# Optimization experiments

Hardware: AMD Instinct MI355X
Metric: run time of the kernel (lower is better)

Reference implementation:

```python
import jax, jax.numpy as jnp
import numpy as np

N, E, F_IN, H, EF, G, GFD = 50000, 800000, 64, 128, 8, 10, 2
NEG_SLOPE = 0.2  # PyG GATv2Conv default negative_slope


def _gatv2_layer(x, src, dst, edge_attr, Wl, bl, Wr, br, We, att, bias):
    # PyG GATv2Conv, heads=1, concat=True, share_weights=False
    n = x.shape[0]
    xl = x @ Wl + bl            # source transform [N,H]
    xr = x @ Wr + br            # target transform [N,H]
    e = edge_attr @ We          # edge embedding   [E,H]
    s = jax.nn.leaky_relu(xl[src] + xr[dst] + e, NEG_SLOPE)  # [E,H]
    logits = s @ att            # [E]
    # numerically-stable segment softmax over destination nodes
    mx = jax.ops.segment_max(logits, dst, num_segments=n)
    mx = jnp.where(jnp.isfinite(mx), mx, 0.0)
    ex = jnp.exp(logits - mx[dst])
    den = jax.ops.segment_sum(ex, dst, num_segments=n)
    alpha = ex / jnp.maximum(den[dst], 1e-16)
    out = jax.ops.segment_sum(alpha[:, None] * xl[src], dst, num_segments=n)
    return out + bias


def _forward(x, edge_index, edge_attr, graph_features, num_graphs, params, head_W, head_b):
    src, dst = edge_index[0], edge_index[1]
    for (Wl, bl, Wr, br, We, att, bias) in params:
        x = jax.nn.relu(_gatv2_layer(x, src, dst, edge_attr, Wl, bl, Wr, br, We, att, bias))
        # dropout p=0.0 / eval mode: no-op
    n_nodes = x.shape[0] // num_graphs
    # faithful replication of the torch reshape chain (graph_feature_dim == 2):
    # graph_features.T [GFD,G] -> unsqueeze(2) -> repeat to [GFD,G,Np] -> view(G,GFD,Np)
    # -> cat(unbind(0), dim=1) -> [GFD, G*Np]
    gf = jnp.broadcast_to(graph_features.T[:, :, None], (GFD, num_graphs, n_nodes))
    gf = gf.reshape(num_graphs, GFD, n_nodes)
    gf = gf.transpose(1, 0, 2).reshape(GFD, num_graphs * n_nodes)
    x = jnp.concatenate([x, gf.T], axis=1)  # [N, H+GFD]
    return x @ head_W + head_b


def setup_inputs():
    key = jax.random.key(0)
    ks = list(jax.random.split(key, 32))
    p = lambda k, s: jax.random.normal(k, s, jnp.float32) * 0.05
    inp = {
        'x': jax.random.normal(ks[0], (N, F_IN), jnp.float32),
        'edge_index': jax.random.randint(ks[1], (2, E), 0, N),
        'edge_attr': jax.random.normal(ks[2], (E, EF), jnp.float32),
        'graph_features': jax.random.normal(ks[3], (G, GFD), jnp.float32),
        'num_graphs': G,
    }
    i = 4
    for l in range(3):
        fin = F_IN if l == 0 else H
        inp[f'Wl{l}'] = p(ks[i], (fin, H)); i += 1
        inp[f'bl{l}'] = jnp.zeros((H,), jnp.float32)
        inp[f'Wr{l}'] = p(ks[i], (fin, H)); i += 1
        inp[f'br{l}'] = jnp.zeros((H,), jnp.float32)
        inp[f'We{l}'] = p(ks[i], (EF, H)); i += 1
        inp[f'att{l}'] = p(ks[i], (H,)); i += 1
        inp[f'bias{l}'] = jnp.zeros((H,), jnp.float32)
    inp['head_W'] = p(ks[i], (H + GFD, 1))
    inp['head_b'] = jnp.zeros((1,), jnp.float32)
    return inp


def reference(x, edge_index, edge_attr, graph_features, num_graphs,
              Wl0, bl0, Wr0, br0, We0, att0, bias0,
              Wl1, bl1, Wr1, br1, We1, att1, bias1,
              Wl2, bl2, Wr2, br2, We2, att2, bias2,
              head_W, head_b):
    params = [(Wl0, bl0, Wr0, br0, We0, att0, bias0),
              (Wl1, bl1, Wr1, br1, We1, att1, bias1),
              (Wl2, bl2, Wr2, br2, We2, att2, bias2)]
    return _forward(x, edge_index, edge_attr, graph_features, num_graphs, params, head_W, head_b)
```

## Files before the change

kernel.cpp:

```cpp
#include <hip/hip_runtime.h>
#include <hip/hip_bf16.h>
#include <math.h>

#define NN 50000
#define EE 800000
#define F_IN 64
#define HH 128
#define EF 8
#define GG 10
#define GFD 2
#define NEG_SLOPE 0.2f
#define NB 64

typedef float v2f __attribute__((ext_vector_type(2)));
__device__ __forceinline__ v2f fma2(v2f a, v2f b, v2f c) {
  return __builtin_elementwise_fma(a, b, c);
}
__device__ __forceinline__ v2f bc2(float x) { v2f r; r.x = x; r.y = x; return r; }

__device__ __forceinline__ float lrelu1(float x) {
  return fmaxf(x, NEG_SLOPE * x);
}

template <int CTRL>
__device__ __forceinline__ float dpp_add(float v) {
  int p = __builtin_amdgcn_update_dpp(0, __float_as_int(v), CTRL, 0xf, 0xf, true);
  return v + __int_as_float(p);
}
__device__ __forceinline__ float red32(float v) {
  v = dpp_add<0xB1>(v);
  v = dpp_add<0x4E>(v);
  v = dpp_add<0x141>(v);
  v = dpp_add<0x140>(v);
  v += __int_as_float(__builtin_amdgcn_ds_swizzle(__float_as_int(v), 0x401F));
  return v;
}

__device__ __forceinline__ void lin2_body(
    int bid, const float* __restrict__ x, int fin,
    const float* __restrict__ Wl, const float* __restrict__ bl,
    const float* __restrict__ Wr, const float* __restrict__ br,
    float* __restrict__ xl, float* __restrict__ xr, int n_nodes) {
  __shared__ float xs[64 * 128];
  const int tid = threadIdx.x;
  const int base = bid * 64;
  int nrows = n_nodes - base; if (nrows > 64) nrows = 64;

  const int total4 = (nrows * fin) >> 2;
  const float4* xsrc = (const float4*)(x + (size_t)base * fin);
  float4* xd = (float4*)xs;
  for (int i = tid; i < total4; i += 256) xd[i] = xsrc[i];
  __syncthreads();

  const int lane = tid & 63;
  const int w = tid >> 6;
  const int c = lane * 2;

  float accl0[16], accl1[16], accr0[16], accr1[16];
#pragma unroll
  for (int j = 0; j < 16; j++) { accl0[j]=0.f; accl1[j]=0.f; accr0[j]=0.f; accr1[j]=0.f; }

  const float* xrow = xs + (w * 16) * fin;
  for (int k = 0; k < fin; k += 4) {
    float2 wl0 = *(const float2*)(Wl + (size_t)k * HH + c);
    float2 wl1 = *(const float2*)(Wl + (size_t)(k + 1) * HH + c);
    float2 wl2 = *(const float2*)(Wl + (size_t)(k + 2) * HH + c);
    float2 wl3 = *(const float2*)(Wl + (size_t)(k + 3) * HH + c);
    float2 wr0 = *(const float2*)(Wr + (size_t)k * HH + c);
    float2 wr1 = *(const float2*)(Wr + (size_t)(k + 1) * HH + c);
    float2 wr2 = *(const float2*)(Wr + (size_t)(k + 2) * HH + c);
    float2 wr3 = *(const float2*)(Wr + (size_t)(k + 3) * HH + c);
#pragma unroll
    for (int j = 0; j < 16; j++) {
      float4 xv = *(const float4*)(xrow + j * fin + k);
      accl0[j] = fmaf(xv.x, wl0.x, accl0[j]);
      accl1[j] = fmaf(xv.x, wl0.y, accl1[j]);
      accr0[j] = fmaf(xv.x, wr0.x, accr0[j]);
      accr1[j] = fmaf(xv.x, wr0.y, accr1[j]);
      accl0[j] = fmaf(xv.y, wl1.x, accl0[j]);
      accl1[j] = fmaf(xv.y, wl1.y, accl1[j]);
      accr0[j] = fmaf(xv.y, wr1.x, accr0[j]);
      accr1[j] = fmaf(xv.y, wr1.y, accr1[j]);
      accl0[j] = fmaf(xv.z, wl2.x, accl0[j]);
      accl1[j] = fmaf(xv.z, wl2.y, accl1[j]);
      accr0[j] = fmaf(xv.z, wr2.x, accr0[j]);
      accr1[j] = fmaf(xv.z, wr2.y, accr1[j]);
      accl0[j] = fmaf(xv.w, wl3.x, accl0[j]);
      accl1[j] = fmaf(xv.w, wl3.y, accl1[j]);
      accr0[j] = fmaf(xv.w, wr3.x, accr0[j]);
      accr1[j] = fmaf(xv.w, wr3.y, accr1[j]);
    }
  }
  float2 blv = *(const float2*)(bl + c);
  float2 brv = *(const float2*)(br + c);
#pragma unroll
  for (int j = 0; j < 16; j++) {
    int n = base + w * 16 + j;
    if (n < n_nodes) {
      *(float2*)(xl + (size_t)n * HH + c) = make_float2(accl0[j] + blv.x, accl1[j] + blv.y);
      *(float2*)(xr + (size_t)n * HH + c) = make_float2(accr0[j] + brv.x, accr1[j] + brv.y);
    }
  }
}

__global__ __launch_bounds__(256) void lin2_kernel(
    const float* __restrict__ x, int fin,
    const float* __restrict__ Wl, const float* __restrict__ bl,
    const float* __restrict__ Wr, const float* __restrict__ br,
    float* __restrict__ xl, float* __restrict__ xr, int n_nodes) {
  lin2_body(blockIdx.x, x, fin, Wl, bl, Wr, br, xl, xr, n_nodes);
}

__device__ __forceinline__ void hist_body(int bid, const int* __restrict__ dst,
                                          int* __restrict__ hist, int ne) {
  int i = bid * 256 + threadIdx.x;
  if (i < ne) atomicAdd(&hist[dst[i]], 1);
}

__global__ __launch_bounds__(256) void fusedA_kernel(
    int nl2, const float* __restrict__ x, int fin,
    const float* __restrict__ Wl, const float* __restrict__ bl,
    const float* __restrict__ Wr, const float* __restrict__ br,
    float* __restrict__ xl, float* __restrict__ xr, int n_nodes,
    const int* __restrict__ dst, int* __restrict__ hist, int ne) {
  if ((int)blockIdx.x < nl2)
    lin2_body(blockIdx.x, x, fin, Wl, bl, Wr, br, xl, xr, n_nodes);
  else
    hist_body(blockIdx.x - nl2, dst, hist, ne);
}

__global__ __launch_bounds__(1024) void reduce_kernel(const int* __restrict__ hist,
                                                      int* __restrict__ bsum, int n) {
  __shared__ int wsum[16];
  const int tid = threadIdx.x;
  const int lane = tid & 63, w = tid >> 6;
  int i = blockIdx.x * 1024 + tid;
  int v = (i < n) ? hist[i] : 0;
#pragma unroll
  for (int off = 32; off; off >>= 1) v += __shfl_xor(v, off);
  if (lane == 0) wsum[w] = v;
  __syncthreads();
  if (tid < 16) {
    int s = wsum[tid];
#pragma unroll
    for (int off = 8; off; off >>= 1) s += __shfl_xor(s, off);
    if (tid == 0) bsum[blockIdx.x] = s;
  }
}

__global__ __launch_bounds__(64) void scanb_kernel(const int* __restrict__ bsum,
                                                   int* __restrict__ bbase,
                                                   int* __restrict__ offs, int nb, int n) {
  const int tid = threadIdx.x;
  int v = (tid < nb) ? bsum[tid] : 0;
  int inc = v;
#pragma unroll
  for (int d = 1; d < 64; d <<= 1) {
    int t2 = __shfl_up(inc, d);
    if (tid >= d) inc += t2;
  }
  if (tid < nb) bbase[tid] = inc - v;
  if (tid == 63) offs[n] = inc;
}

__global__ __launch_bounds__(1024) void scanc_kernel(const int* __restrict__ hist,
                                                     const int* __restrict__ bbase,
                                                     int* __restrict__ offs,
                                                     int* __restrict__ cursor, int n) {
  __shared__ int wsum[16], wpre[16];
  const int tid = threadIdx.x;
  const int lane = tid & 63, w = tid >> 6;
  int i = blockIdx.x * 1024 + tid;
  int orig = (i < n) ? hist[i] : 0;
  int v = orig;
#pragma unroll
  for (int d = 1; d < 64; d <<= 1) {
    int t2 = __shfl_up(v, d);
    if (lane >= d) v += t2;
  }
  if (lane == 63) wsum[w] = v;
  __syncthreads();
  if (tid < 16) {
    int s = wsum[tid];
    int inc = s;
#pragma unroll
    for (int d = 1; d < 16; d <<= 1) {
      int t2 = __shfl_up(inc, d);
      if (tid >= d) inc += t2;
    }
    wpre[tid] = inc - s;
  }
  __syncthreads();
  if (i < n) {
    int ex = bbase[blockIdx.x] + wpre[w] + (v - orig);
    offs[i] = ex; cursor[i] = ex;
  }
}

__device__ __forceinline__ void scatter_body(
    int bid, const int* __restrict__ src, const int* __restrict__ dst,
    int* __restrict__ cursor, int* __restrict__ pk,
    const float4* __restrict__ ea4, float4* __restrict__ eas, int ne) {
  int i = bid * 256 + threadIdx.x;
  if (i < ne) {
    int d = dst[i];
    int pos = atomicAdd(&cursor[d], 1);
    pk[pos] = src[i] * 512;
    float4 a = ea4[i * 2], b = ea4[i * 2 + 1];
    eas[pos * 2] = a; eas[pos * 2 + 1] = b;
  }
}

__device__ __forceinline__ void deg_hist_body(int bid, const int* __restrict__ offs,
                                              int* __restrict__ hist2, int n) {
  __shared__ int lhist[NB];
  const int tid = threadIdx.x;
  int i = bid * 256 + tid;
  if (tid < NB) lhist[tid] = 0;
  __syncthreads();
  if (i < n) {
    int d = offs[i + 1] - offs[i];
    int key = NB - 1 - min(d, NB - 1);
    atomicAdd(&lhist[key], 1);
  }
  __syncthreads();
  if (tid < NB && lhist[tid]) atomicAdd(&hist2[tid], lhist[tid]);
}

__global__ __launch_bounds__(256) void fusedB_kernel(
    int nsc, const int* __restrict__ src, const int* __restrict__ dst,
    int* __restrict__ cursor, int* __restrict__ pk,
    const float4* __restrict__ ea4, float4* __restrict__ eas, int ne,
    const int* __restrict__ offs, int* __restrict__ hist2, int n) {
  if ((int)blockIdx.x < nsc)
    scatter_body(blockIdx.x, src, dst, cursor, pk, ea4, eas, ne);
  else
    deg_hist_body(blockIdx.x - nsc, offs, hist2, n);
}

__global__ __launch_bounds__(64) void scan64_kernel(const int* __restrict__ hist2,
                                                    int* __restrict__ cursor2) {
  const int tid = threadIdx.x;
  int v = hist2[tid];
  int inc = v;
#pragma unroll
  for (int d = 1; d < 64; d <<= 1) {
    int t2 = __shfl_up(inc, d);
    if (tid >= d) inc += t2;
  }
  cursor2[tid] = inc - v;
}

__global__ __launch_bounds__(256) void deg_scatter_kernel(const int* __restrict__ offs,
                                                          int* __restrict__ cursor2,
                                                          int4* __restrict__ meta4, int n) {
  __shared__ int lhist[NB];
  __shared__ int lbase[NB];
  const int tid = threadIdx.x;
  int i = blockIdx.x * 256 + tid;
  if (tid < NB) lhist[tid] = 0;
  __syncthreads();
  int key = 0, rank = 0, bb = 0, ee = 0;
  const bool valid = (i < n);
  if (valid) {
    bb = offs[i]; ee = offs[i + 1];
    int d = ee - bb;
    key = NB - 1 - min(d, NB - 1);
    rank = atomicAdd(&lhist[key], 1);
  }
  __syncthreads();
  if (tid < NB && lhist[tid]) lbase[tid] = atomicAdd(&cursor2[tid], lhist[tid]);
  __syncthreads();
  if (valid) meta4[lbase[key] + rank] = make_int4(bb, ee, i, 0);
}

__global__ __launch_bounds__(256, 4) void gat_fused_kernel(
    const float* __restrict__ xl, const float* __restrict__ xr,
    const float* __restrict__ eas, const float* __restrict__ We,
    const float* __restrict__ att,
    const int* __restrict__ pk, const int4* __restrict__ meta4,
    const float* __restrict__ bias,
    float* __restrict__ xout, int n_nodes,
    float* __restrict__ out_head, const float* __restrict__ hw,
    const float* __restrict__ hb) {
  const int lane = threadIdx.x & 63;
  const int g = lane >> 5, t = lane & 31;
  const int c = t * 4;
  const int tb = t * 16;
  const int nwaves = gridDim.x * 4;

  v2f wea[EF], web[EF];
#pragma unroll
  for (int k = 0; k < EF; k++) {
    float4 w4 = *(const float4*)(We + k * HH + c);
    wea[k].x = w4.x; wea[k].y = w4.y;
    web[k].x = w4.z; web[k].y = w4.w;
  }
  const float4 at = *(const float4*)(att + c);
  const float4 bi = *(const float4*)(bias + c);
  const char* xlb = (const char*)xl;
  const char* easb = (const char*)eas;
  float4 hwv = make_float4(0.f, 0.f, 0.f, 0.f);
  float hw0 = 0.f, hw1 = 0.f, hb0 = 0.f;
  if (out_head) {
    hwv = *(const float4*)(hw + c);
    hw0 = hw[HH]; hw1 = hw[HH + 1]; hb0 = hb[0];
  }

  int wid = blockIdx.x * 4 + (threadIdx.x >> 6);
  if (wid >= n_nodes) return;
  int4 mt = meta4[wid];
  float4 vr4 = *(const float4*)(xr + (size_t)mt.z * HH + c);

  while (true) {
    const int b = mt.x, e = mt.y, node = mt.z;
    const int deg = e - b;
    const int nwid = wid + nwaves;
    const bool hasN = nwid < n_nodes;
    int4 mtN = mt;
    if (hasN) mtN = meta4[nwid];

    v2f vra; vra.x = vr4.x; vra.y = vr4.y;
    v2f vrb; vrb.x = vr4.z; vrb.y = vr4.w;

    float4 o;
    if (deg == 0) {
      o.x = fmaxf(bi.x, 0.f); o.y = fmaxf(bi.y, 0.f);
      o.z = fmaxf(bi.z, 0.f); o.w = fmaxf(bi.w, 0.f);
    } else {
      const int emax = e - 1;
      v2f acc0 = bc2(0.f), acc1 = bc2(0.f);
      float den = 0.f;
      v2f vlAa, vlAb, epA0, epA1, eqA0, eqA1;
      v2f vlBa, vlBb, epB0, epB1, eqB0, eqB1;

#define LOADS(VLa, VLb, P0, P1, Q0, Q1, IDX)                        \
  do {                                                              \
    int _cx = min((IDX), emax);                                     \
    float4 _ep = *(const float4*)(easb + (_cx << 5));               \
    float4 _eq = *(const float4*)(easb + (_cx << 5) + 16);          \
    int _ob = pk[_cx];                                              \
    float4 _vl = *(const float4*)(xlb + (_ob + tb));                \
    P0.x = _ep.x; P0.y = _ep.y; P1.x = _ep.z; P1.y = _ep.w;         \
    Q0.x = _eq.x; Q0.y = _eq.y; Q1.x = _eq.z; Q1.y = _eq.w;         \
    VLa.x = _vl.x; VLa.y = _vl.y; VLb.x = _vl.z; VLb.y = _vl.w;     \
  } while (0)

#define PROCESS(VLa, VLb, P0, P1, Q0, Q1, IDX)                       \
  do {                                                               \
    v2f s0 = VLa + vra;                                              \
    v2f s1 = VLb + vrb;                                              \
    s0 = fma2(bc2(P0.x), wea[0], s0); s1 = fma2(bc2(P0.x), web[0], s1); \
    s0 = fma2(bc2(P0.y), wea[1], s0); s1 = fma2(bc2(P0.y), web[1], s1); \
    s0 = fma2(bc2(P1.x), wea[2], s0); s1 = fma2(bc2(P1.x), web[2], s1); \
    s0 = fma2(bc2(P1.y), wea[3], s0); s1 = fma2(bc2(P1.y), web[3], s1); \
    s0 = fma2(bc2(Q0.x), wea[4], s0); s1 = fma2(bc2(Q0.x), web[4], s1); \
    s0 = fma2(bc2(Q0.y), wea[5], s0); s1 = fma2(bc2(Q0.y), web[5], s1); \
    s0 = fma2(bc2(Q1.x), wea[6], s0); s1 = fma2(bc2(Q1.x), web[6], s1); \
    s0 = fma2(bc2(Q1.y), wea[7], s0); s1 = fma2(bc2(Q1.y), web[7], s1); \
    v2f m0 = s0 * bc2(NEG_SLOPE);                                    \
    v2f m1 = s1 * bc2(NEG_SLOPE);                                    \
    float l0 = fmaxf(s0.x, m0.x), l1 = fmaxf(s0.y, m0.y);            \
    float l2 = fmaxf(s1.x, m1.x), l3 = fmaxf(s1.y, m1.y);            \
    float v = l0 * at.x;                                             \
    v = fmaf(l1, at.y, v);                                           \
    v = fmaf(l2, at.z, v);                                           \
    v = fmaf(l3, at.w, v);                                           \
    v = red32(v);                                                    \
    const float p = ((IDX) < e) ? __expf(v) : 0.f;                   \
    den += p;                                                        \
    acc0 = fma2(bc2(p), VLa, acc0);                                  \
    acc1 = fma2(bc2(p), VLb, acc1);                                  \
  } while (0)

      int idx = b + g;
      LOADS(vlAa, vlAb, epA0, epA1, eqA0, eqA1, idx);
      LOADS(vlBa, vlBb, epB0, epB1, eqB0, eqB1, idx + 2);

      const int nit = (deg + 3) >> 2;
      for (int j = 0; j < nit; j++) {
        PROCESS(vlAa, vlAb, epA0, epA1, eqA0, eqA1, idx);
        LOADS(vlAa, vlAb, epA0, epA1, eqA0, eqA1, idx + 4);
        PROCESS(vlBa, vlBb, epB0, epB1, eqB0, eqB1, idx + 2);
        LOADS(vlBa, vlBb, epB0, epB1, eqB0, eqB1, idx + 6);
        idx += 4;
      }
#undef LOADS
#undef PROCESS

      den += __shfl_xor(den, 32);
      float a0 = acc0.x + __shfl_xor(acc0.x, 32);
      float a1 = acc0.y + __shfl_xor(acc0.y, 32);
      float a2 = acc1.x + __shfl_xor(acc1.x, 32);
      float a3 = acc1.y + __shfl_xor(acc1.y, 32);

      const float inv = 1.f / fmaxf(den, 1e-16f);
      o.x = fmaxf(fmaf(a0, inv, bi.x), 0.f);
      o.y = fmaxf(fmaf(a1, inv, bi.y), 0.f);
      o.z = fmaxf(fmaf(a2, inv, bi.z), 0.f);
      o.w = fmaxf(fmaf(a3, inv, bi.w), 0.f);
    }

    float4 vrN = vr4;
    if (hasN) vrN = *(const float4*)(xr + (size_t)mtN.z * HH + c);

    if (!out_head) {
      if (g == 0) *(float4*)(xout + (size_t)node * HH + c) = o;
    } else {
      float hv = o.x * hwv.x + o.y * hwv.y + o.z * hwv.z + o.w * hwv.w;
      hv = red32(hv);
      if (lane == 0) {
        int k = node / (NN / GG);
        int i0 = 2 * k, i1 = 2 * k + 1;
        float gf0 = xout[(i0 % GG) * GFD + (i0 / GG)];
        float gf1 = xout[(i1 % GG) * GFD + (i1 / GG)];
        out_head[node] = hv + gf0 * hw0 + gf1 * hw1 + hb0;
      }
    }

    if (!hasN) break;
    wid = nwid; mt = mtN; vr4 = vrN;
  }
}

extern "C" void kernel_launch(void* const* d_in, const int* in_sizes, int n_in,
                              void* d_out, int out_size, void* d_ws, size_t ws_size,
                              hipStream_t stream) {
  const float* x_in = (const float*)d_in[0];
  const int*   eidx = (const int*)d_in[1];
  const float* ea   = (const float*)d_in[2];
  const float* gf   = (const float*)d_in[3];
  const int* src = eidx;
  const int* dst = eidx + EE;
  const float* head_W = (const float*)d_in[26];
  const float* head_b = (const float*)d_in[27];
  float* out = (float*)d_out;

  const int NCHUNK = (NN + 1023) / 1024;
  const int NL2B = (NN + 63) / 64;
  const int NHB  = (EE + 255) / 256;
  const int NDB  = (NN + 255) / 256;

  float* P      = (float*)d_ws;
  float* Q      = P + (size_t)NN * HH;
  float* R      = Q + (size_t)NN * HH;
  float* eas    = R + (size_t)NN * HH;
  int*   pk     = (int*)(eas + (size_t)EE * EF);
  int*   hist   = pk + EE;
  int*   hist2  = hist + NN;
  int*   offs   = hist2 + NB;
  int*   cursor = offs + NN + 1;
  int*   cursor2= cursor + NN;
  int*   bsum   = cursor2 + NB;
  int*   bbase  = bsum + NCHUNK;
  int4*  meta4  = (int4*)(((size_t)(bbase + NCHUNK) + 15) & ~(size_t)15);

  const float* Wl0 = (const float*)d_in[5], *bl0 = (const float*)d_in[6];
  const float* Wr0 = (const float*)d_in[7], *br0 = (const float*)d_in[8];

  (void)hipMemsetAsync(hist, 0, (NN + NB) * sizeof(int), stream);
  fusedA_kernel<<<NL2B + NHB, 256, 0, stream>>>(NL2B, x_in, F_IN, Wl0, bl0, Wr0, br0,
                                                P, Q, NN, dst, hist, EE);
  reduce_kernel<<<NCHUNK, 1024, 0, stream>>>(hist, bsum, NN);
  scanb_kernel<<<1, 64, 0, stream>>>(bsum, bbase, offs, NCHUNK, NN);
  scanc_kernel<<<NCHUNK, 1024, 0, stream>>>(hist, bbase, offs, cursor, NN);
  fusedB_kernel<<<NHB + NDB, 256, 0, stream>>>(NHB, src, dst, cursor, pk,
                                               (const float4*)ea, (float4*)eas, EE,
                                               offs, hist2, NN);
  scan64_kernel<<<1, 64, 0, stream>>>(hist2, cursor2);
  deg_scatter_kernel<<<NDB, 256, 0, stream>>>(offs, cursor2, meta4, NN);

  for (int l = 0; l < 3; l++) {
    const float* We   = (const float*)d_in[5 + 7 * l + 4];
    const float* att  = (const float*)d_in[5 + 7 * l + 5];
    const float* bias = (const float*)d_in[5 + 7 * l + 6];

    if (l > 0) {
      const float* Wl = (const float*)d_in[5 + 7 * l + 0];
      const float* bl = (const float*)d_in[5 + 7 * l + 1];
      const float* Wr = (const float*)d_in[5 + 7 * l + 2];
      const float* br = (const float*)d_in[5 + 7 * l + 3];
      lin2_kernel<<<NL2B, 256, 0, stream>>>(R, HH, Wl, bl, Wr, br, P, Q, NN);
    }
    if (l < 2) {
      gat_fused_kernel<<<2048, 256, 0, stream>>>(P, Q, eas, We, att, pk, meta4,
                                                 bias, R, NN, nullptr, nullptr, nullptr);
    } else {
      gat_fused_kernel<<<2048, 256, 0, stream>>>(P, Q, eas, We, att, pk, meta4,
                                                 bias, (float*)gf, NN, out, head_W, head_b);
    }
  }
}
```

Before: 482.7 us.

## Replace degree-sorted node schedule with edge-balanced contiguous node ranges per wave

Drops the degree histogram, scan and degree-bucketed node permutation (two kernels plus a meta array). Instead, each of 8192 waves binary-searches the CSR offsets to get a contiguous node range covering an equal share of edges, then walks nodes in order. This removes two preprocessing launches and gives sequential access to offsets, xr and the edge arrays. The cost is that a wave's nodes can have very mixed degrees, so the longest-first ordering that balanced the tail is lost.

```diff
diff --git a/kernel.cpp b/kernel.cpp
--- a/kernel.cpp
+++ b/kernel.cpp
@@ -10,17 +10,13 @@
 #define GG 10
 #define GFD 2
 #define NEG_SLOPE 0.2f
-#define NB 64
+#define NWV 8192
 
 typedef float v2f __attribute__((ext_vector_type(2)));
 __device__ __forceinline__ v2f fma2(v2f a, v2f b, v2f c) {
   return __builtin_elementwise_fma(a, b, c);
 }
 __device__ __forceinline__ v2f bc2(float x) { v2f r; r.x = x; r.y = x; return r; }
-
-__device__ __forceinline__ float lrelu1(float x) {
-  return fmaxf(x, NEG_SLOPE * x);
-}
 
 template <int CTRL>
 __device__ __forceinline__ float dpp_add(float v) {
@@ -211,75 +207,36 @@
   }
 }
 
-__device__ __forceinline__ void deg_hist_body(int bid, const int* __restrict__ offs,
-                                              int* __restrict__ hist2, int n) {
-  __shared__ int lhist[NB];
-  const int tid = threadIdx.x;
-  int i = bid * 256 + tid;
-  if (tid < NB) lhist[tid] = 0;
-  __syncthreads();
-  if (i < n) {
-    int d = offs[i + 1] - offs[i];
-    int key = NB - 1 - min(d, NB - 1);
-    atomicAdd(&lhist[key], 1);
-  }
-  __syncthreads();
-  if (tid < NB && lhist[tid]) atomicAdd(&hist2[tid], lhist[tid]);
+__device__ __forceinline__ void wbounds_body(int bid, const int* __restrict__ offs,
+                                             int* __restrict__ wstart, int n, int ne) {
+  int i = bid * 256 + threadIdx.x;
+  if (i > NWV) return;
+  long long tgt = (long long)i * ne / NWV;
+  int lo = 0, hi = n;
+  while (lo < hi) {
+    int mid = (lo + hi) >> 1;
+    if ((long long)offs[mid + 1] > tgt) hi = mid; else lo = mid + 1;
+  }
+  wstart[i] = lo;
 }
 
 __global__ __launch_bounds__(256) void fusedB_kernel(
     int nsc, const int* __restrict__ src, const int* __restrict__ dst,
     int* __restrict__ cursor, int* __restrict__ pk,
     const float4* __restrict__ ea4, float4* __restrict__ eas, int ne,
-    const int* __restrict__ offs, int* __restrict__ hist2, int n) {
+    const int* __restrict__ offs, int* __restrict__ wstart, int n) {
   if ((int)blockIdx.x < nsc)
     scatter_body(blockIdx.x, src, dst, cursor, pk, ea4, eas, ne);
   else
-    deg_hist_body(blockIdx.x - nsc, offs, hist2, n);
-}
-
-__global__ __launch_bounds__(64) void scan64_kernel(const int* __restrict__ hist2,
-                                                    int* __restrict__ cursor2) {
-  const int tid = threadIdx.x;
-  int v = hist2[tid];
-  int inc = v;
-#pragma unroll
-  for (int d = 1; d < 64; d <<= 1) {
-    int t2 = __shfl_up(inc, d);
-    if (tid >= d) inc += t2;
-  }
-  cursor2[tid] = inc - v;
-}
-
-__global__ __launch_bounds__(256) void deg_scatter_kernel(const int* __restrict__ offs,
-                                                          int* __restrict__ cursor2,
-                                                          int4* __restrict__ meta4, int n) {
-  __shared__ int lhist[NB];
-  __shared__ int lbase[NB];
-  const int tid = threadIdx.x;
-  int i = blockIdx.x * 256 + tid;
-  if (tid < NB) lhist[tid] = 0;
-  __syncthreads();
-  int key = 0, rank = 0, bb = 0, ee = 0;
-  const bool valid = (i < n);
-  if (valid) {
-    bb = offs[i]; ee = offs[i + 1];
-    int d = ee - bb;
-    key = NB - 1 - min(d, NB - 1);
-    rank = atomicAdd(&lhist[key], 1);
-  }
-  __syncthreads();
-  if (tid < NB && lhist[tid]) lbase[tid] = atomicAdd(&cursor2[tid], lhist[tid]);
-  __syncthreads();
-  if (valid) meta4[lbase[key] + rank] = make_int4(bb, ee, i, 0);
+    wbounds_body(blockIdx.x - nsc, offs, wstart, n, ne);
 }
 
 __global__ __launch_bounds__(256, 4) void gat_fused_kernel(
     const float* __restrict__ xl, const float* __restrict__ xr,
     const float* __restrict__ eas, const float* __restrict__ We,
     const float* __restrict__ att,
-    const int* __restrict__ pk, const int4* __restrict__ meta4,
-    const float* __restrict__ bias,
+    const int* __restrict__ pk, const int* __restrict__ offs,
+    const int* __restrict__ wstart, const float* __restrict__ bias,
     float* __restrict__ xout, int n_nodes,
     float* __restrict__ out_head, const float* __restrict__ hw,
     const float* __restrict__ hb) {
@@ -287,7 +244,7 @@
   const int g = lane >> 5, t = lane & 31;
   const int c = t * 4;
   const int tb = t * 16;
-  const int nwaves = gridDim.x * 4;
+  const int w = blockIdx.x * 4 + (threadIdx.x >> 6);
 
   v2f wea[EF], web[EF];
 #pragma unroll
@@ -307,18 +264,15 @@
     hw0 = hw[HH]; hw1 = hw[HH + 1]; hb0 = hb[0];
   }
 
-  int wid = blockIdx.x * 4 + (threadIdx.x >> 6);
-  if (wid >= n_nodes) return;
-  int4 mt = meta4[wid];
-  float4 vr4 = *(const float4*)(xr + (size_t)mt.z * HH + c);
+  int node = wstart[w];
+  const int nend = wstart[w + 1];
+  if (node >= nend) return;
+  int b = offs[node];
+  int e = offs[node + 1];
+  float4 vr4 = *(const float4*)(xr + (size_t)node * HH + c);
 
   while (true) {
-    const int b = mt.x, e = mt.y, node = mt.z;
     const int deg = e - b;
-    const int nwid = wid + nwaves;
-    const bool hasN = nwid < n_nodes;
-    int4 mtN = mt;
-    if (hasN) mtN = meta4[nwid];
 
     v2f vra; vra.x = vr4.x; vra.y = vr4.y;
     v2f vrb; vrb.x = vr4.z; vrb.y = vr4.w;
@@ -337,8 +291,8 @@
 #define LOADS(VLa, VLb, P0, P1, Q0, Q1, IDX)                        \
   do {                                                              \
     int _cx = min((IDX), emax);                                     \
-    float4 _ep = *(const float4*)(easb + (_cx << 5));               \
-    float4 _eq = *(const float4*)(easb + (_cx << 5) + 16);          \
+    float4 _ep = *(const float4*)(easb + ((long)_cx << 5));         \
+    float4 _eq = *(const float4*)(easb + ((long)_cx << 5) + 16);    \
     int _ob = pk[_cx];                                              \
     float4 _vl = *(const float4*)(xlb + (_ob + tb));                \
     P0.x = _ep.x; P0.y = _ep.y; P1.x = _ep.z; P1.y = _ep.w;         \
@@ -401,8 +355,14 @@
       o.w = fmaxf(fmaf(a3, inv, bi.w), 0.f);
     }
 
+    const int nodeN = node + 1;
+    const bool hasN = nodeN < nend;
+    int eN = e;
     float4 vrN = vr4;
-    if (hasN) vrN = *(const float4*)(xr + (size_t)mtN.z * HH + c);
+    if (hasN) {
+      eN = offs[nodeN + 1];
+      vrN = *(const float4*)(xr + (size_t)nodeN * HH + c);
+    }
 
     if (!out_head) {
       if (g == 0) *(float4*)(xout + (size_t)node * HH + c) = o;
@@ -419,7 +379,7 @@
     }
 
     if (!hasN) break;
-    wid = nwid; mt = mtN; vr4 = vrN;
+    node = nodeN; b = e; e = eN; vr4 = vrN;
   }
 }
 
@@ -439,7 +399,7 @@
   const int NCHUNK = (NN + 1023) / 1024;
   const int NL2B = (NN + 63) / 64;
   const int NHB  = (EE + 255) / 256;
-  const int NDB  = (NN + 255) / 256;
+  const int NWB  = (NWV + 1 + 255) / 256;
 
   float* P      = (float*)d_ws;
   float* Q      = P + (size_t)NN * HH;
@@ -447,28 +407,24 @@
   float* eas    = R + (size_t)NN * HH;
   int*   pk     = (int*)(eas + (size_t)EE * EF);
   int*   hist   = pk + EE;
-  int*   hist2  = hist + NN;
-  int*   offs   = hist2 + NB;
+  int*   offs   = hist + NN;
   int*   cursor = offs + NN + 1;
-  int*   cursor2= cursor + NN;
-  int*   bsum   = cursor2 + NB;
+  int*   bsum   = cursor + NN;
   int*   bbase  = bsum + NCHUNK;
-  int4*  meta4  = (int4*)(((size_t)(bbase + NCHUNK) + 15) & ~(size_t)15);
+  int*   wstart = bbase + NCHUNK;
 
   const float* Wl0 = (const float*)d_in[5], *bl0 = (const float*)d_in[6];
   const float* Wr0 = (const float*)d_in[7], *br0 = (const float*)d_in[8];
 
-  (void)hipMemsetAsync(hist, 0, (NN + NB) * sizeof(int), stream);
+  (void)hipMemsetAsync(hist, 0, NN * sizeof(int), stream);
   fusedA_kernel<<<NL2B + NHB, 256, 0, stream>>>(NL2B, x_in, F_IN, Wl0, bl0, Wr0, br0,
                                                 P, Q, NN, dst, hist, EE);
   reduce_kernel<<<NCHUNK, 1024, 0, stream>>>(hist, bsum, NN);
   scanb_kernel<<<1, 64, 0, stream>>>(bsum, bbase, offs, NCHUNK, NN);
   scanc_kernel<<<NCHUNK, 1024, 0, stream>>>(hist, bbase, offs, cursor, NN);
-  fusedB_kernel<<<NHB + NDB, 256, 0, stream>>>(NHB, src, dst, cursor, pk,
+  fusedB_kernel<<<NHB + NWB, 256, 0, stream>>>(NHB, src, dst, cursor, pk,
                                                (const float4*)ea, (float4*)eas, EE,
-                                               offs, hist2, NN);
-  scan64_kernel<<<1, 64, 0, stream>>>(hist2, cursor2);
-  deg_scatter_kernel<<<NDB, 256, 0, stream>>>(offs, cursor2, meta4, NN);
+                                               offs, wstart, NN);
 
   for (int l = 0; l < 3; l++) {
     const float* We   = (const float*)d_in[5 + 7 * l + 4];
@@ -483,11 +439,13 @@
       lin2_kernel<<<NL2B, 256, 0, stream>>>(R, HH, Wl, bl, Wr, br, P, Q, NN);
     }
     if (l < 2) {
-      gat_fused_kernel<<<2048, 256, 0, stream>>>(P, Q, eas, We, att, pk, meta4,
-                                                 bias, R, NN, nullptr, nullptr, nullptr);
+      gat_fused_kernel<<<NWV / 4, 256, 0, stream>>>(P, Q, eas, We, att, pk, offs,
+                                                    wstart, bias, R, NN,
+                                                    nullptr, nullptr, nullptr);
     } else {
-      gat_fused_kernel<<<2048, 256, 0, stream>>>(P, Q, eas, We, att, pk, meta4,
-                                                 bias, (float*)gf, NN, out, head_W, head_b);
-    }
-  }
-}
+      gat_fused_kernel<<<NWV / 4, 256, 0, stream>>>(P, Q, eas, We, att, pk, offs,
+                                                    wstart, bias, (float*)gf, NN,
+                                                    out, head_W, head_b);
+    }
+  }
+}
```

New measurement: 492.2 us. Within noise of the previous version (+2.0%).
